# Performance work log

Hardware: AMD Instinct MI355X
Metric: run time of the kernel (lower is better)

## Reference

```python
import jax, jax.numpy as jnp
import numpy as np

# Config (matches init_kwargs): complex RG-LRU, sigmoid gates, gate_a_imag='same',
# fixed input norm, log_a_scale=-8.0
B, S, D_IN = 4, 4096, 1024
D_HID = 2048            # merged (real|imag) hidden width
D_INNER = D_HID // 2    # complex channels
NB = 8                  # n_diag_blocks
LOG_A_SCALE = -8.0
R_MIN, R_MAX = 0.9, 0.999


def _bdl(x, w, b):
    """BlockDiagonalLinear: x (B,S,d_in) -> (B,S,nb*bout). w: (nb,bin,bout), b: (nb*bout,)."""
    Bb, Ss, d = x.shape
    nb, bin_, bout = w.shape
    xb = x.reshape(Bb, Ss, nb, bin_)
    y = jnp.einsum('bsni,nio->bsno', xb, w) + b.reshape(nb, bout)
    return y.reshape(Bb, Ss, nb * bout)


def setup_inputs() -> dict:
    key = jax.random.key(0)
    ks = jax.random.split(key, 10)
    x = jax.random.normal(ks[0], (B, S, D_IN), dtype=jnp.float32)
    # input Dense(d_hidden)
    w_in = jax.random.normal(ks[1], (D_IN, D_HID), dtype=jnp.float32) / np.sqrt(D_IN)
    b_in = jnp.zeros((D_HID,), jnp.float32)
    # BlockDiagonalLinear weights for gate_x and gate_a
    bin_, bout = D_HID // NB, D_INNER // NB
    w_gx = jax.random.normal(ks[2], (NB, bin_, bout), dtype=jnp.float32) / np.sqrt(bin_)
    b_gx = jnp.zeros((D_INNER,), jnp.float32)
    w_ga = jax.random.normal(ks[3], (NB, bin_, bout), dtype=jnp.float32) / np.sqrt(bin_)
    b_ga = jnp.zeros((D_INNER,), jnp.float32)
    # stable_init_real: softplus(param) = -0.5*log(u*(rmax^2-rmin^2)+rmin^2)
    u = jax.random.uniform(ks[4], (D_INNER,))
    a_real = 0.5 * jnp.log(u * (R_MAX**2 - R_MIN**2) + R_MIN**2 + 1e-8)
    a_real_param = jnp.log(jnp.exp(-a_real) - 1.0)
    # stable_init_imag: pi * init_maxval_imag * u, init_maxval_imag = 0.1
    a_imag_param = jnp.pi * 0.1 * jax.random.uniform(ks[5], (D_INNER,))
    # output Dense(d_in)
    w_out = jax.random.normal(ks[6], (D_HID, D_IN), dtype=jnp.float32) / np.sqrt(D_HID)
    b_out = jnp.zeros((D_IN,), jnp.float32)
    return dict(x=x, w_in=w_in, b_in=b_in, w_gx=w_gx, b_gx=b_gx, w_ga=w_ga,
                b_ga=b_ga, a_real_param=a_real_param, a_imag_param=a_imag_param,
                w_out=w_out, b_out=b_out)


def reference(x, w_in, b_in, w_gx, b_gx, w_ga, b_ga, a_real_param, a_imag_param,
              w_out, b_out):
    xh = x @ w_in + b_in                                  # (B,S,D_HID)
    gate_x = jax.nn.sigmoid(_bdl(xh, w_gx, b_gx))         # (B,S,D_INNER)
    gate_a = jax.nn.sigmoid(_bdl(xh, w_ga, b_ga))         # (B,S,D_INNER)
    # log_a = scale * gate_a_real * softplus(a_real_param)  (negative => |a|<1)
    log_a = LOG_A_SCALE * gate_a * jax.nn.softplus(a_real_param)
    log_a_imag = a_imag_param * gate_a                    # gate_a_imag = 'same'
    a = jnp.exp(jax.lax.complex(log_a, log_a_imag))       # complex decay (B,S,D_INNER)
    # merged_to_complex: first half real, second half imag
    xc = jax.lax.complex(xh[..., :D_INNER], xh[..., D_INNER:])
    xc = gate_x * xc
    # fixed input norm: sqrt(1 - |a|^2) = sqrt(1 - exp(2*log_a))
    norm = jnp.sqrt(jnp.maximum(1.0 - jnp.exp(2.0 * log_a), 1e-6))
    xc = norm * xc
    # linear recurrence h_t = a_t*h_{t-1} + x_t via parallel associative scan
    def combine(l, r):
        return (r[0] * l[0], r[0] * l[1] + r[1])
    _, h = jax.lax.associative_scan(combine, (a, xc), axis=1)  # h0 = 0
    h_m = jnp.concatenate([h.real, h.imag], axis=-1)      # complex_to_merged (B,S,D_HID)
    y = h_m @ w_out + b_out                               # (B,S,D_IN)
    h_last = h_m[:, -1]                                   # (B,D_HID)
    return y, h_last
```

## Files before the change

### kernel.cpp

```cpp
#include <hip/hip_runtime.h>
#include <cstdint>
#include <cstddef>

typedef short bf16x8 __attribute__((ext_vector_type(8)));
typedef ushort ushort8 __attribute__((ext_vector_type(8)));
typedef float f32x4 __attribute__((ext_vector_type(4)));

__device__ __forceinline__ float b2f(ushort u) {
    union { float f; uint32_t i; } v; v.i = ((uint32_t)u) << 16; return v.f;
}
__device__ __forceinline__ ushort f2b(float f) {
    union { float f; uint32_t i; } v; v.f = f;
    uint32_t r = v.i + 0x7FFFu + ((v.i >> 16) & 1u);
    return (ushort)(r >> 16);
}

#define ASYNC16(g, l) \
    __builtin_amdgcn_global_load_lds((const __attribute__((address_space(1))) void*)(g), \
                                     (__attribute__((address_space(3))) void*)(l), 16, 0, 0)

__global__ void cvt_x_kernel(const float4* __restrict__ x, ushort4* __restrict__ xb) {
    int i = blockIdx.x * 256 + threadIdx.x;
    float4 v = x[i];
    ushort4 o; o.x = f2b(v.x); o.y = f2b(v.y); o.z = f2b(v.z); o.w = f2b(v.w);
    xb[i] = o;
}

__global__ void transpose_cvt(const float* __restrict__ in, ushort* __restrict__ out,
                              int R, int C, int outStride,
                              size_t inBatch, size_t outBatch) {
    __shared__ float t[64 * 65];
    const int tid = threadIdx.x;
    const int r0 = blockIdx.y * 64, c0 = blockIdx.x * 64;
    const float* inp = in + blockIdx.z * inBatch;
    ushort* outp = out + blockIdx.z * outBatch;

    const int lr = tid >> 4;
    const int lc = (tid & 15) * 4;
#pragma unroll
    for (int i = 0; i < 4; ++i) {
        const int row = lr + i * 16;
        const float4 v = *(const float4*)&inp[(size_t)(r0 + row) * C + c0 + lc];
        t[row * 65 + lc + 0] = v.x;
        t[row * 65 + lc + 1] = v.y;
        t[row * 65 + lc + 2] = v.z;
        t[row * 65 + lc + 3] = v.w;
    }
    __syncthreads();
    const int oc = tid >> 2;
    const int orr = (tid & 3) * 16;
    ushort8 a, b;
#pragma unroll
    for (int i = 0; i < 8; ++i) a[i] = f2b(t[(orr + i) * 65 + oc]);
#pragma unroll
    for (int i = 0; i < 8; ++i) b[i] = f2b(t[(orr + 8 + i) * 65 + oc]);
    ushort* dst = outp + (size_t)(c0 + oc) * outStride + r0 + orr;
    *(ushort8*)dst = a;
    *(ushort8*)(dst + 8) = b;
}

__global__ void prep_small_kernel(const float* __restrict__ b_gx, const float* __restrict__ b_ga,
                                  const float* __restrict__ arp,
                                  float* __restrict__ bg, float* __restrict__ sp) {
    int idx = blockIdx.x * 256 + threadIdx.x;
    {
        int nb = idx >> 8, r = idx & 255;
        bg[idx] = (r < 128) ? b_gx[nb * 128 + r] : b_ga[nb * 128 + r - 128];
    }
    if (idx < 1024) sp[idx] = log1pf(__expf(arp[idx]));
}

template<int EPI>
__launch_bounds__(256, 2)
__global__ void gemm_bt(const ushort* __restrict__ A, const ushort* __restrict__ B,
                        int M, int N, int K, int lda, int ldb, int gxbits,
                        const float* __restrict__ bias,
                        float* __restrict__ o0,
                        ushort* __restrict__ ob) {
    __shared__ ushort At[128 * 32];
    __shared__ ushort Bt[128 * 32];
    const int tid = threadIdx.x;
    const int lane = tid & 63;
    const int wave = tid >> 6;
    const int wr = wave >> 1, wc = wave & 1;

    const int swz = (blockIdx.x & 7) * (gridDim.x >> 3) + (blockIdx.x >> 3);
    const int m0 = (swz >> gxbits) * 128;
    const int n0 = (swz & ((1 << gxbits) - 1)) * 128;

    const ushort* Ab = A;
    if (EPI == 1) Ab += (size_t)(n0 >> 8) * 256;

    const int arow = tid >> 2;
    const int acolb = (tid & 3) << 4;
    const char* ag0 = (const char*)Ab + ((size_t)(m0 + arow) * lda) * 2 + acolb;
    const char* ag1 = ag0 + (size_t)64 * lda * 2;
    const char* bgp0 = (const char*)B + ((size_t)(n0 + arow) * ldb) * 2 + acolb;
    const char* bgp1 = bgp0 + (size_t)64 * ldb * 2;
    ushort* la0 = At + tid * 8; ushort* la1 = la0 + 2048;
    ushort* lb0 = Bt + tid * 8; ushort* lb1 = lb0 + 2048;

    f32x4 acc[4][4];
#pragma unroll
    for (int i = 0; i < 4; ++i)
#pragma unroll
        for (int j = 0; j < 4; ++j) acc[i][j] = (f32x4){0.f, 0.f, 0.f, 0.f};

    const int fm = lane & 15;
    const int fko = (lane >> 4) * 8;
    const ushort* Af = At + (wr * 64 + fm) * 32 + fko;
    const ushort* Bf = Bt + (wc * 64 + fm) * 32 + fko;

    const int nk = K >> 5;
    for (int kk = 0; kk < nk; ++kk) {
        __syncthreads();
        const size_t off = (size_t)kk * 64;
        ASYNC16(ag0 + off, la0);
        ASYNC16(ag1 + off, la1);
        ASYNC16(bgp0 + off, lb0);
        ASYNC16(bgp1 + off, lb1);
        __syncthreads();
        bf16x8 af[4], bfv[4];
#pragma unroll
        for (int i = 0; i < 4; ++i) af[i]  = *(const bf16x8*)(Af + i * 512);
#pragma unroll
        for (int i = 0; i < 4; ++i) bfv[i] = *(const bf16x8*)(Bf + i * 512);
#pragma unroll
        for (int i = 0; i < 4; ++i)
#pragma unroll
            for (int j = 0; j < 4; ++j)
                acc[i][j] = __builtin_amdgcn_mfma_f32_16x16x32_bf16(af[i], bfv[j], acc[i][j], 0, 0, 0);
    }

    const int r0 = (lane >> 4) * 4;
    const int cn = lane & 15;
#pragma unroll
    for (int j = 0; j < 4; ++j) {
        const int n = n0 + wc * 64 + j * 16 + cn;
        const float bv = bias[n];
        if (EPI == 1) {
            const int nb = n >> 8, rr = n & 255;
            const int c = nb * 128 + (rr & 127);
            const int wh = (rr >> 7) & 1;
#pragma unroll
            for (int i = 0; i < 4; ++i) {
                const int mb = m0 + wr * 64 + i * 16 + r0;
#pragma unroll
                for (int r = 0; r < 4; ++r) {
                    float v = acc[i][j][r] + bv;
                    ob[(size_t)(mb + r) * 2048 + c * 2 + wh] = f2b(1.f / (1.f + __expf(-v)));
                }
            }
        } else if (EPI == 0) {
#pragma unroll
            for (int i = 0; i < 4; ++i) {
                const int mb = m0 + wr * 64 + i * 16 + r0;
#pragma unroll
                for (int r = 0; r < 4; ++r)
                    ob[(size_t)(mb + r) * N + n] = f2b(acc[i][j][r] + bv);
            }
        } else {
#pragma unroll
            for (int i = 0; i < 4; ++i) {
                const int mb = m0 + wr * 64 + i * 16 + r0;
#pragma unroll
                for (int r = 0; r < 4; ++r)
                    o0[(size_t)(mb + r) * N + n] = acc[i][j][r] + bv;
            }
        }
    }
}

template<int FINAL>
__global__ void scan_chunk(const ushort2* __restrict__ gxga,
                           ushort* __restrict__ xhb,
                           const float* __restrict__ sp, const float* __restrict__ aim,
                           float2* __restrict__ carryA, float2* __restrict__ carryH,
                           const float2* __restrict__ prefixH,
                           float* __restrict__ hlast) {
    const int c = blockIdx.y * 256 + threadIdx.x;
    const int b = blockIdx.z;
    const int chunk = blockIdx.x;
    const int m0 = b * 4096 + chunk * 64;
    const float spc = sp[c], amc = aim[c];
    float Ar = 1.f, Ai = 0.f, Hr = 0.f, Hi = 0.f;
    if (FINAL) { float2 p = prefixH[chunk * 4096 + b * 1024 + c]; Hr = p.x; Hi = p.y; }
#pragma unroll 8
    for (int t = 0; t < 64; ++t) {
        const size_t m = (size_t)(m0 + t);
        const ushort2 g = gxga[m * 1024 + c];
        const float xr = b2f(xhb[m * 2048 + c]);
        const float xi = b2f(xhb[m * 2048 + c + 1024]);
        const float gav = b2f(g.y);
        const float er = __expf(-8.f * gav * spc);
        float sn, cs; __sincosf(amc * gav, &sn, &cs);
        const float f = sqrtf(fmaxf(1.f - er * er, 1e-6f)) * b2f(g.x);
        const float ar = er * cs, ai = er * sn;
        const float xcr = f * xr, xci = f * xi;
        const float h2 = ar * Hr - ai * Hi + xcr;
        Hi = ar * Hi + ai * Hr + xci; Hr = h2;
        if (FINAL) {
            xhb[m * 2048 + c] = f2b(Hr);
            xhb[m * 2048 + c + 1024] = f2b(Hi);
        } else {
            const float a2 = ar * Ar - ai * Ai; Ai = ar * Ai + ai * Ar; Ar = a2;
        }
    }
    if (!FINAL) {
        const int s = chunk * 4096 + b * 1024 + c;
        carryA[s] = make_float2(Ar, Ai);
        carryH[s] = make_float2(Hr, Hi);
    } else if (chunk == 63) {
        hlast[b * 2048 + c] = Hr;
        hlast[b * 2048 + c + 1024] = Hi;
    }
}

__global__ void scan_top(const float2* __restrict__ cA, const float2* __restrict__ cH,
                         float2* __restrict__ pH) {
    const int s = blockIdx.x * 256 + threadIdx.x;
    float pr = 0.f, pi = 0.f;
    for (int ch = 0; ch < 64; ++ch) {
        pH[ch * 4096 + s] = make_float2(pr, pi);
        float2 A = cA[ch * 4096 + s];
        float2 H = cH[ch * 4096 + s];
        float t = A.x * pr - A.y * pi + H.x;
        pi = A.x * pi + A.y * pr + H.y;
        pr = t;
    }
}

__global__ void ws_report_kernel(float* out, float code) {
    out[blockIdx.x * 256 + threadIdx.x] = code;
}

extern "C" void kernel_launch(void* const* d_in, const int* in_sizes, int n_in,
                              void* d_out, int out_size, void* d_ws, size_t ws_size,
                              hipStream_t stream) {
    const float* x     = (const float*)d_in[0];
    const float* w_in  = (const float*)d_in[1];
    const float* b_in  = (const float*)d_in[2];
    const float* w_gx  = (const float*)d_in[3];
    const float* b_gx  = (const float*)d_in[4];
    const float* w_ga  = (const float*)d_in[5];
    const float* b_ga  = (const float*)d_in[6];
    const float* arp   = (const float*)d_in[7];
    const float* aip   = (const float*)d_in[8];
    const float* w_out = (const float*)d_in[9];
    const float* b_out = (const float*)d_in[10];
    float* out = (float*)d_out;

    char* p = (char*)d_ws;
    ushort* R0    = (ushort*)p; p += 67108864;
    ushort* xb    = R0;
    ushort* gxga  = R0;
    ushort* xhb   = (ushort*)p; p += 67108864;
    ushort* w_inT = (ushort*)p; p += 4194304;
    ushort* w_outT= (ushort*)p; p += 4194304;
    ushort* WgT   = (ushort*)p; p += 1048576;
    float*  bg    = (float*)p;  p += 8192;
    float*  sp    = (float*)p;  p += 4096;
    float2* cA    = (float2*)p; p += 2097152;
    float2* cH    = (float2*)p; p += 2097152;
    float2* pH    = (float2*)p; p += 2097152;
    size_t need = (size_t)(p - (char*)d_ws);
    if (ws_size < need) {
        float code = 1000.0f + (float)(ws_size >> 20);
        ws_report_kernel<<<64, 256, 0, stream>>>(out, code);
        return;
    }

    cvt_x_kernel<<<16384, 256, 0, stream>>>((const float4*)x, (ushort4*)xb);
    transpose_cvt<<<dim3(32, 16, 1), 256, 0, stream>>>(w_in, w_inT, 1024, 2048, 1024, 0, 0);
    transpose_cvt<<<dim3(16, 32, 1), 256, 0, stream>>>(w_out, w_outT, 2048, 1024, 2048, 0, 0);
    transpose_cvt<<<dim3(2, 4, 8), 256, 0, stream>>>(w_gx, WgT, 256, 128, 256, 32768, 65536);
    transpose_cvt<<<dim3(2, 4, 8), 256, 0, stream>>>(w_ga, WgT + 32768, 256, 128, 256, 32768, 65536);
    prep_small_kernel<<<8, 256, 0, stream>>>(b_gx, b_ga, arp, bg, sp);

    gemm_bt<0><<<2048, 256, 0, stream>>>(xb, w_inT, 16384, 2048, 1024, 1024, 1024, 4,
                                         b_in, nullptr, xhb);
    gemm_bt<1><<<2048, 256, 0, stream>>>(xhb, WgT, 16384, 2048, 256, 2048, 256, 4,
                                         bg, nullptr, gxga);
    scan_chunk<0><<<dim3(64, 4, 4), 256, 0, stream>>>((const ushort2*)gxga, xhb, sp, aip,
                                                      cA, cH, nullptr, nullptr);
    scan_top<<<16, 256, 0, stream>>>(cA, cH, pH);
    scan_chunk<1><<<dim3(64, 4, 4), 256, 0, stream>>>((const ushort2*)gxga, xhb, sp, aip,
                                                      nullptr, nullptr, pH, out + 16777216);
    gemm_bt<2><<<1024, 256, 0, stream>>>(xhb, w_outT, 16384, 1024, 2048, 2048, 2048, 3,
                                         b_out, out, nullptr);
}
```

Measured before the change: 417.9 us.

## Add 256x256-tile 512-thread GEMM with 4-stage async LDS pipeline for dense projections

Introduces a new GEMM kernel using 256x256 output tiles, 8 waves, and a four-deep ring of global_load_lds buffers with explicit vmcnt waits, and uses it for the input and output dense projections. Larger tiles raise arithmetic intensity and reduce global/L2 traffic per FLOP, while the deeper prefetch hides load latency. In exchange it uses 128KB LDS and many accumulator registers, so only one block fits per CU, and the output-projection grid shrinks to 256 blocks, which may leave some of the 256 CUs with poor wave-level latency hiding.

```diff
diff --git a/kernel.cpp b/kernel.cpp
--- a/kernel.cpp
+++ b/kernel.cpp
@@ -68,6 +68,101 @@
         bg[idx] = (r < 128) ? b_gx[nb * 128 + r] : b_ga[nb * 128 + r - 128];
     }
     if (idx < 1024) sp[idx] = log1pf(__expf(arp[idx]));
+}
+
+template<int EPI>
+__launch_bounds__(512, 1)
+__global__ void gemm256(const ushort* __restrict__ A, const ushort* __restrict__ B,
+                        int M, int N, int K, int lda, int ldb, int gxbits,
+                        const float* __restrict__ bias,
+                        float* __restrict__ o0, ushort* __restrict__ ob) {
+    __shared__ ushort lds[4 * 16384];
+    const int tid = threadIdx.x;
+    const int lane = tid & 63;
+    const int wave = tid >> 6;
+    const int wr = wave >> 2;
+    const int wc = wave & 3;
+
+    const int swz = (blockIdx.x & 7) * (gridDim.x >> 3) + (blockIdx.x >> 3);
+    const int m0 = (swz >> gxbits) * 256;
+    const int n0 = (swz & ((1 << gxbits) - 1)) * 256;
+
+    const int rA = tid >> 2;
+    const int cA = (tid & 3) ^ ((rA >> 1) & 3);
+    const char* aSrc0 = (const char*)A + 2 * ((size_t)(m0 + rA) * lda + cA * 8);
+    const char* aSrc1 = aSrc0 + 2 * (size_t)128 * lda;
+    const char* bSrc0 = (const char*)B + 2 * ((size_t)(n0 + rA) * ldb + cA * 8);
+    const char* bSrc1 = bSrc0 + 2 * (size_t)128 * ldb;
+
+    f32x4 acc[8][4];
+#pragma unroll
+    for (int i = 0; i < 8; ++i)
+#pragma unroll
+        for (int j = 0; j < 4; ++j) acc[i][j] = (f32x4){0.f, 0.f, 0.f, 0.f};
+
+    const int fphys = (lane >> 4) ^ (((lane & 15) >> 1) & 3);
+    const int baseA = (wr * 128 + (lane & 15)) * 32 + fphys * 8;
+    const int baseB = 8192 + (wc * 64 + (lane & 15)) * 32 + fphys * 8;
+
+    const int nt = K >> 5;
+
+#define STAGE256(t) do {                                               \
+        ushort* buf = lds + ((t) & 3) * 16384;                         \
+        const size_t o = (size_t)(t) * 64;                             \
+        ASYNC16(aSrc0 + o, buf + tid * 8);                             \
+        ASYNC16(aSrc1 + o, buf + tid * 8 + 4096);                      \
+        ASYNC16(bSrc0 + o, buf + 8192 + tid * 8);                      \
+        ASYNC16(bSrc1 + o, buf + 8192 + tid * 8 + 4096);               \
+    } while (0)
+
+    STAGE256(0); STAGE256(1); STAGE256(2);
+    asm volatile("s_waitcnt vmcnt(8)" ::: "memory");
+    __builtin_amdgcn_s_barrier();
+    __builtin_amdgcn_sched_barrier(0);
+
+    for (int t = 0; t < nt; ++t) {
+        const int rem = nt - 1 - t;
+        if (rem >= 3) STAGE256(t + 3);
+        const ushort* buf = lds + (t & 3) * 16384;
+        bf16x8 af[8], bf[4];
+#pragma unroll
+        for (int mf = 0; mf < 8; ++mf) af[mf] = *(const bf16x8*)(buf + baseA + mf * 512);
+#pragma unroll
+        for (int nf = 0; nf < 4; ++nf) bf[nf] = *(const bf16x8*)(buf + baseB + nf * 512);
+        __builtin_amdgcn_s_setprio(1);
+#pragma unroll
+        for (int mf = 0; mf < 8; ++mf)
+#pragma unroll
+            for (int nf = 0; nf < 4; ++nf)
+                acc[mf][nf] = __builtin_amdgcn_mfma_f32_16x16x32_bf16(af[mf], bf[nf], acc[mf][nf], 0, 0, 0);
+        __builtin_amdgcn_s_setprio(0);
+        if (rem > 0) {
+            if (rem >= 3)      asm volatile("s_waitcnt vmcnt(8)" ::: "memory");
+            else if (rem == 2) asm volatile("s_waitcnt vmcnt(4)" ::: "memory");
+            else               asm volatile("s_waitcnt vmcnt(0)" ::: "memory");
+            __builtin_amdgcn_s_barrier();
+            __builtin_amdgcn_sched_barrier(0);
+        }
+    }
+#undef STAGE256
+
+    const int r0 = (lane >> 4) * 4;
+    const int cn = lane & 15;
+#pragma unroll
+    for (int nf = 0; nf < 4; ++nf) {
+        const int col = n0 + wc * 64 + nf * 16 + cn;
+        const float bv = bias[col];
+#pragma unroll
+        for (int mf = 0; mf < 8; ++mf) {
+            const int rowb = m0 + wr * 128 + mf * 16 + r0;
+#pragma unroll
+            for (int r = 0; r < 4; ++r) {
+                const float v = acc[mf][nf][r] + bv;
+                if (EPI == 0) ob[(size_t)(rowb + r) * N + col] = f2b(v);
+                else          o0[(size_t)(rowb + r) * N + col] = v;
+            }
+        }
+    }
 }
 
 template<int EPI>
@@ -150,14 +245,6 @@
                     float v = acc[i][j][r] + bv;
                     ob[(size_t)(mb + r) * 2048 + c * 2 + wh] = f2b(1.f / (1.f + __expf(-v)));
                 }
-            }
-        } else if (EPI == 0) {
-#pragma unroll
-            for (int i = 0; i < 4; ++i) {
-                const int mb = m0 + wr * 64 + i * 16 + r0;
-#pragma unroll
-                for (int r = 0; r < 4; ++r)
-                    ob[(size_t)(mb + r) * N + n] = f2b(acc[i][j][r] + bv);
             }
         } else {
 #pragma unroll
@@ -277,8 +364,8 @@
     transpose_cvt<<<dim3(2, 4, 8), 256, 0, stream>>>(w_ga, WgT + 32768, 256, 128, 256, 32768, 65536);
     prep_small_kernel<<<8, 256, 0, stream>>>(b_gx, b_ga, arp, bg, sp);
 
-    gemm_bt<0><<<2048, 256, 0, stream>>>(xb, w_inT, 16384, 2048, 1024, 1024, 1024, 4,
-                                         b_in, nullptr, xhb);
+    gemm256<0><<<512, 512, 0, stream>>>(xb, w_inT, 16384, 2048, 1024, 1024, 1024, 3,
+                                        b_in, nullptr, xhb);
     gemm_bt<1><<<2048, 256, 0, stream>>>(xhb, WgT, 16384, 2048, 256, 2048, 256, 4,
                                          bg, nullptr, gxga);
     scan_chunk<0><<<dim3(64, 4, 4), 256, 0, stream>>>((const ushort2*)gxga, xhb, sp, aip,
@@ -286,6 +373,6 @@
     scan_top<<<16, 256, 0, stream>>>(cA, cH, pH);
     scan_chunk<1><<<dim3(64, 4, 4), 256, 0, stream>>>((const ushort2*)gxga, xhb, sp, aip,
                                                       nullptr, nullptr, pH, out + 16777216);
-    gemm_bt<2><<<1024, 256, 0, stream>>>(xhb, w_outT, 16384, 1024, 2048, 2048, 2048, 3,
-                                         b_out, out, nullptr);
-}
+    gemm256<2><<<256, 512, 0, stream>>>(xhb, w_outT, 16384, 1024, 2048, 2048, 2048, 2,
+                                        b_out, out, nullptr);
+}
```

Result: no change. 413.3 us (-1.1%).

## Replace input/output GEMMs with 256x256-tile 8-wave pipelined MFMA kernel

Applied to the files above, without the earlier changes.

Adds a new GEMM kernel with 256x256 output tiles, 512 threads (8 waves), a 128KB double-buffered LDS with XOR-swizzled async global-to-LDS loads, and interleaved MFMA phases that use barriers and setprio. It is used for the input projection and the output projection, replacing the 128x128 gemm_bt for those two GEMMs. The aim is more operand reuse per LDS byte and overlap of loads with MFMA work. In exchange it runs one block per CU with high register pressure, and the output GEMM gets only 256 blocks, which risks poor CU fill and tail effects.

```diff
diff --git a/kernel.cpp b/kernel.cpp
--- a/kernel.cpp
+++ b/kernel.cpp
@@ -68,6 +68,149 @@
         bg[idx] = (r < 128) ? b_gx[nb * 128 + r] : b_ga[nb * 128 + r - 128];
     }
     if (idx < 1024) sp[idx] = log1pf(__expf(arp[idx]));
+}
+
+#define MFMA1(a_, x_, y_) a_ = __builtin_amdgcn_mfma_f32_16x16x32_bf16(x_, y_, a_, 0, 0, 0)
+#define VM4() asm volatile("s_waitcnt vmcnt(4)" ::: "memory")
+#define VM0() asm volatile("s_waitcnt vmcnt(0)" ::: "memory")
+#define PRE() do { __builtin_amdgcn_s_barrier(); \
+    asm volatile("s_waitcnt lgkmcnt(0)" ::: "memory"); \
+    __builtin_amdgcn_sched_barrier(0); __builtin_amdgcn_s_setprio(1); } while (0)
+#define POST() do { __builtin_amdgcn_s_setprio(0); __builtin_amdgcn_s_barrier(); \
+    __builtin_amdgcn_sched_barrier(0); } while (0)
+
+template<int EPI>
+__launch_bounds__(512, 1)
+__global__ void gemm8p(const ushort* __restrict__ A, const ushort* __restrict__ B,
+                       int M, int N, int K, int lda, int ldb, int gxbits,
+                       const float* __restrict__ bias,
+                       float* __restrict__ o0, ushort* __restrict__ ob) {
+    __shared__ ushort lds[65536];
+    const int tid = threadIdx.x;
+    const int lane = tid & 63;
+    const int wave = tid >> 6;
+    const int wr = wave >> 2;
+    const int wc = wave & 3;
+
+    const int swz = (blockIdx.x & 7) * (gridDim.x >> 3) + (blockIdx.x >> 3);
+    const int m0 = (swz >> gxbits) * 256;
+    const int n0 = (swz & ((1 << gxbits) - 1)) * 256;
+
+    const int srow = tid >> 3;
+    const int schk = (tid & 7) ^ (srow & 7);
+    const char* aS = (const char*)A + 2 * ((size_t)(m0 + srow) * lda) + schk * 16;
+    const char* bS = (const char*)B + 2 * ((size_t)(n0 + srow) * ldb) + schk * 16;
+    const size_t astep = (size_t)64 * lda * 2;
+    const size_t bstep = (size_t)64 * ldb * 2;
+
+#define STG_A0(t) do { size_t cb = (size_t)(t) * 128; ushort* d = lds + ((t) & 1) * 32768; \
+        ASYNC16(aS + cb, d + tid * 8); ASYNC16(aS + astep + cb, d + 4096 + tid * 8); } while (0)
+#define STG_A1(t) do { size_t cb = (size_t)(t) * 128; ushort* d = lds + ((t) & 1) * 32768 + 8192; \
+        ASYNC16(aS + 2 * astep + cb, d + tid * 8); ASYNC16(aS + 3 * astep + cb, d + 4096 + tid * 8); } while (0)
+#define STG_B0(t) do { size_t cb = (size_t)(t) * 128; ushort* d = lds + ((t) & 1) * 32768 + 16384; \
+        ASYNC16(bS + cb, d + tid * 8); ASYNC16(bS + bstep + cb, d + 4096 + tid * 8); } while (0)
+#define STG_B1(t) do { size_t cb = (size_t)(t) * 128; ushort* d = lds + ((t) & 1) * 32768 + 24576; \
+        ASYNC16(bS + 2 * bstep + cb, d + tid * 8); ASYNC16(bS + 3 * bstep + cb, d + 4096 + tid * 8); } while (0)
+
+    f32x4 acc[8][4];
+#pragma unroll
+    for (int i = 0; i < 8; ++i)
+#pragma unroll
+        for (int j = 0; j < 4; ++j) acc[i][j] = (f32x4){0.f, 0.f, 0.f, 0.f};
+
+    const int cph0 = (((lane >> 4)) ^ (lane & 7)) * 8;
+    const int cph1 = (((lane >> 4) + 4) ^ (lane & 7)) * 8;
+    const int aRB = (wr * 128 + (lane & 15)) * 64;
+    const int bRB = 16384 + (wc * 64 + (lane & 15)) * 64;
+
+    bf16x8 aa[8], p0, p1, p2, p3, q0, q1, q2, q3;
+
+#define LDA(bb, mfb) do { _Pragma("unroll") \
+    for (int i_ = 0; i_ < 4; ++i_) { \
+        aa[2 * i_]     = *(const bf16x8*)(lds + (bb) + aRB + ((mfb) + i_) * 1024 + cph0); \
+        aa[2 * i_ + 1] = *(const bf16x8*)(lds + (bb) + aRB + ((mfb) + i_) * 1024 + cph1); \
+    } } while (0)
+#define LDP(bb) do { \
+        p0 = *(const bf16x8*)(lds + (bb) + bRB + cph0); \
+        p1 = *(const bf16x8*)(lds + (bb) + bRB + cph1); \
+        p2 = *(const bf16x8*)(lds + (bb) + bRB + 1024 + cph0); \
+        p3 = *(const bf16x8*)(lds + (bb) + bRB + 1024 + cph1); } while (0)
+#define LDQ(bb) do { \
+        q0 = *(const bf16x8*)(lds + (bb) + bRB + 2048 + cph0); \
+        q1 = *(const bf16x8*)(lds + (bb) + bRB + 2048 + cph1); \
+        q2 = *(const bf16x8*)(lds + (bb) + bRB + 3072 + cph0); \
+        q3 = *(const bf16x8*)(lds + (bb) + bRB + 3072 + cph1); } while (0)
+#define MMAP(mfb) do { _Pragma("unroll") \
+    for (int i_ = 0; i_ < 4; ++i_) { const int m_ = (mfb) + i_; \
+        MFMA1(acc[m_][0], aa[2 * i_], p0); MFMA1(acc[m_][0], aa[2 * i_ + 1], p1); \
+        MFMA1(acc[m_][1], aa[2 * i_], p2); MFMA1(acc[m_][1], aa[2 * i_ + 1], p3); \
+    } } while (0)
+#define MMAQ(mfb) do { _Pragma("unroll") \
+    for (int i_ = 0; i_ < 4; ++i_) { const int m_ = (mfb) + i_; \
+        MFMA1(acc[m_][2], aa[2 * i_], q0); MFMA1(acc[m_][2], aa[2 * i_ + 1], q1); \
+        MFMA1(acc[m_][3], aa[2 * i_], q2); MFMA1(acc[m_][3], aa[2 * i_ + 1], q3); \
+    } } while (0)
+
+    const int nt = K >> 6;
+    STG_A0(0); STG_A1(0); STG_B0(0); STG_B1(0);
+    STG_A0(1); STG_A1(1);
+    VM4();
+    __builtin_amdgcn_s_barrier();
+    __builtin_amdgcn_sched_barrier(0);
+
+    for (int it = 0; it < (nt >> 1); ++it) {
+        const int t0 = 2 * it;
+        const bool nl = (t0 + 2 < nt);
+        LDA(0, 0); LDP(0);
+        STG_B0(t0 + 1);
+        PRE(); MMAP(0); POST();
+        LDQ(0);
+        STG_B1(t0 + 1);
+        PRE(); MMAQ(0); POST();
+        LDA(0, 4);
+        if (nl) STG_A0(t0 + 2);
+        PRE(); MMAQ(4); POST();
+        if (nl) { STG_A1(t0 + 2); VM4(); } else VM0();
+        PRE(); MMAP(4); POST();
+        LDA(32768, 0); LDP(32768);
+        if (nl) STG_B0(t0 + 2);
+        PRE(); MMAP(0); POST();
+        LDQ(32768);
+        if (nl) STG_B1(t0 + 2);
+        PRE(); MMAQ(0); POST();
+        LDA(32768, 4);
+        if (nl) STG_A0(t0 + 3);
+        PRE(); MMAQ(4); POST();
+        if (nl) { STG_A1(t0 + 3); VM4(); } else VM0();
+        PRE(); MMAP(4); POST();
+    }
+
+    const int r0 = (lane >> 4) * 4;
+    const int cn = lane & 15;
+#pragma unroll
+    for (int nf = 0; nf < 4; ++nf) {
+        const int col = n0 + wc * 64 + nf * 16 + cn;
+        const float bv = bias[col];
+#pragma unroll
+        for (int mf = 0; mf < 8; ++mf) {
+            const int rowb = m0 + wr * 128 + mf * 16 + r0;
+#pragma unroll
+            for (int r = 0; r < 4; ++r) {
+                const float v = acc[mf][nf][r] + bv;
+                if (EPI == 0) ob[(size_t)(rowb + r) * N + col] = f2b(v);
+                else          o0[(size_t)(rowb + r) * N + col] = v;
+            }
+        }
+    }
+#undef STG_A0
+#undef STG_A1
+#undef STG_B0
+#undef STG_B1
+#undef LDA
+#undef LDP
+#undef LDQ
+#undef MMAP
+#undef MMAQ
 }
 
 template<int EPI>
@@ -150,14 +293,6 @@
                     float v = acc[i][j][r] + bv;
                     ob[(size_t)(mb + r) * 2048 + c * 2 + wh] = f2b(1.f / (1.f + __expf(-v)));
                 }
-            }
-        } else if (EPI == 0) {
-#pragma unroll
-            for (int i = 0; i < 4; ++i) {
-                const int mb = m0 + wr * 64 + i * 16 + r0;
-#pragma unroll
-                for (int r = 0; r < 4; ++r)
-                    ob[(size_t)(mb + r) * N + n] = f2b(acc[i][j][r] + bv);
             }
         } else {
 #pragma unroll
@@ -277,8 +412,8 @@
     transpose_cvt<<<dim3(2, 4, 8), 256, 0, stream>>>(w_ga, WgT + 32768, 256, 128, 256, 32768, 65536);
     prep_small_kernel<<<8, 256, 0, stream>>>(b_gx, b_ga, arp, bg, sp);
 
-    gemm_bt<0><<<2048, 256, 0, stream>>>(xb, w_inT, 16384, 2048, 1024, 1024, 1024, 4,
-                                         b_in, nullptr, xhb);
+    gemm8p<0><<<512, 512, 0, stream>>>(xb, w_inT, 16384, 2048, 1024, 1024, 1024, 3,
+                                       b_in, nullptr, xhb);
     gemm_bt<1><<<2048, 256, 0, stream>>>(xhb, WgT, 16384, 2048, 256, 2048, 256, 4,
                                          bg, nullptr, gxga);
     scan_chunk<0><<<dim3(64, 4, 4), 256, 0, stream>>>((const ushort2*)gxga, xhb, sp, aip,
@@ -286,6 +421,6 @@
     scan_top<<<16, 256, 0, stream>>>(cA, cH, pH);
     scan_chunk<1><<<dim3(64, 4, 4), 256, 0, stream>>>((const ushort2*)gxga, xhb, sp, aip,
                                                       nullptr, nullptr, pH, out + 16777216);
-    gemm_bt<2><<<1024, 256, 0, stream>>>(xhb, w_outT, 16384, 1024, 2048, 2048, 2048, 3,
-                                         b_out, out, nullptr);
-}
+    gemm8p<2><<<256, 512, 0, stream>>>(xhb, w_outT, 16384, 1024, 2048, 2048, 2048, 2,
+                                       b_out, out, nullptr);
+}
```

Result: faster. 406.0 us (-2.8%).
